# Performance work log

Measured on AMD Instinct MI355X. Metric: run time of the kernel, lower is better.

## Reference

```python
import jax, jax.numpy as jnp
import numpy as np

B, H, S, DK = 4, 8, 2048, 64

def setup_inputs() -> dict:
    key = jax.random.key(0)
    kq, kk, kv = jax.random.split(key, 3)
    queries = jax.random.normal(kq, (B, H, S, DK), dtype=jnp.float32)
    keys = jax.random.normal(kk, (B, H, S, DK), dtype=jnp.float32)
    values = jax.random.normal(kv, (B, H, S, DK), dtype=jnp.float32)
    # causal mask: 1.0 where attention is disallowed (strictly upper triangular)
    mask = jnp.triu(jnp.ones((S, S), dtype=jnp.float32), k=1)[None, None]
    return {"queries": queries, "keys": keys, "values": values, "dk": DK, "mask": mask}

def reference(queries, keys, values, dk, mask):
    # score: [B, H, S, S]
    score = jnp.einsum("bhqd,bhkd->bhqk", queries, keys) / jnp.sqrt(jnp.float32(dk))
    if mask is not None:
        score = score + mask * -1e9
    attn = jax.nn.softmax(score, axis=-1)
    return jnp.einsum("bhqk,bhkd->bhqd", attn, values)
```

## Files before the change

kernel.cpp:

```cpp
#include <hip/hip_runtime.h>

typedef __attribute__((ext_vector_type(8))) short short8;
typedef __attribute__((ext_vector_type(4))) float f32x4;

#define DEV __device__ __forceinline__

constexpr int S_LEN = 2048;
constexpr int DK_LEN = 64;
constexpr int QBLK = 128;
constexpr int KBLK = 64;
constexpr float QSCALE = 0.18033688011112042f;

constexpr int KHI = 0;
constexpr int KLO = 8192;
constexpr int VHI = 16384;
constexpr int VLO = 24576;
constexpr int PBASE = 32768;
constexpr int LDS_BYTES = 65536;

DEV unsigned int f2bf(float x) {
  unsigned int u = __float_as_uint(x);
  return (u + 0x7fffu + ((u >> 16) & 1u)) >> 16;
}
DEV float bf2f(unsigned int h) { return __uint_as_float(h << 16); }
DEV int swz(int row, int slot) { return slot ^ ((row + (row >> 3)) & 7); }

DEV f32x4 MFMA(short8 a, short8 b, f32x4 c) {
  return __builtin_amdgcn_mfma_f32_16x16x32_bf16(a, b, c, 0, 0, 0);
}

__global__ __launch_bounds__(256, 2)
void fattn_fwd(const float* __restrict__ Qg, const float* __restrict__ Kg,
               const float* __restrict__ Vg, float* __restrict__ Og)
{
  __shared__ char smem[LDS_BYTES];
  const f32x4 vzero = {0.f, 0.f, 0.f, 0.f};
  const int tid = threadIdx.x;
  const int w  = tid >> 6;
  const int ln = tid & 63;
  const int g  = ln >> 4;
  const int c  = ln & 15;
  const int bh = blockIdx.y;
  const int qi = (bh < 16) ? (15 - (int)blockIdx.x) : (int)blockIdx.x;
  const int q0w = qi * QBLK + w * 32;
  const size_t base = (size_t)bh * S_LEN * DK_LEN;
  const float* Qb = Qg + base;
  const float* Kb = Kg + base;
  const float* Vb = Vg + base;

  short8 qfh[2][2], qfl[2][2];
#pragma unroll
  for (int qt = 0; qt < 2; ++qt) {
    const float* Qr = Qb + (size_t)(q0w + 16 * qt + c) * DK_LEN;
#pragma unroll
    for (int kk = 0; kk < 2; ++kk) {
      f32x4 a = *(const f32x4*)(Qr + kk * 32 + 8 * g);
      f32x4 b = *(const f32x4*)(Qr + kk * 32 + 8 * g + 4);
      float x[8];
#pragma unroll
      for (int i = 0; i < 4; ++i) { x[i] = a[i] * QSCALE; x[4 + i] = b[i] * QSCALE; }
#pragma unroll
      for (int i = 0; i < 8; ++i) {
        unsigned int h = f2bf(x[i]);
        unsigned int l = f2bf(x[i] - bf2f(h));
        qfh[qt][kk][i] = (short)h;
        qfl[qt][kk][i] = (short)l;
      }
    }
  }

  f32x4 acc[4][2];
#pragma unroll
  for (int td = 0; td < 4; ++td)
#pragma unroll
    for (int qt = 0; qt < 2; ++qt) acc[td][qt] = vzero;
  float m_r[2]  = {-3e38f, -3e38f};
  float lsum[2] = {0.f, 0.f};

  const int ntiles = 2 * qi + 2;
  for (int kt = 0; kt < ntiles; ++kt) {
    const int kv0 = kt * KBLK;
    __syncthreads();
#pragma unroll
    for (int i = 0; i < 4; ++i) {
      int f = tid + 256 * i;
      int row = f >> 4, c4 = f & 15;
      f32x4 kv = *(const f32x4*)(Kb + (size_t)(kv0 + row) * DK_LEN + c4 * 4);
      unsigned int h[4], l[4];
#pragma unroll
      for (int j = 0; j < 4; ++j) { h[j] = f2bf(kv[j]); l[j] = f2bf(kv[j] - bf2f(h[j])); }
      int byte = row * 128 + swz(row, c4 >> 1) * 16 + (c4 & 1) * 8;
      *(uint2*)(smem + KHI + byte) = make_uint2(h[0] | (h[1] << 16), h[2] | (h[3] << 16));
      *(uint2*)(smem + KLO + byte) = make_uint2(l[0] | (l[1] << 16), l[2] | (l[3] << 16));
    }
#pragma unroll
    for (int it = 0; it < 2; ++it) {
      int p = tid + 256 * it;
      int rp = p >> 4, c4 = p & 15;
      const float* vp = Vb + (size_t)(kv0 + 2 * rp) * DK_LEN + c4 * 4;
      f32x4 v0 = *(const f32x4*)(vp);
      f32x4 v1 = *(const f32x4*)(vp + DK_LEN);
#pragma unroll
      for (int j = 0; j < 4; ++j) {
        int d = 4 * c4 + j;
        unsigned int h0 = f2bf(v0[j]), h1 = f2bf(v1[j]);
        unsigned int l0 = f2bf(v0[j] - bf2f(h0)), l1 = f2bf(v1[j] - bf2f(h1));
        int byte = d * 128 + swz(d, rp >> 2) * 16 + (rp & 3) * 4;
        *(unsigned int*)(smem + VHI + byte) = h0 | (h1 << 16);
        *(unsigned int*)(smem + VLO + byte) = l0 | (l1 << 16);
      }
    }
    __syncthreads();

    if (kv0 > q0w + 31) continue;
    const bool need_mask = (kv0 + KBLK - 1) > q0w;

    f32x4 sv[2][4];
#pragma unroll
    for (int qt = 0; qt < 2; ++qt)
#pragma unroll
      for (int t = 0; t < 4; ++t) sv[qt][t] = vzero;
#pragma unroll
    for (int t = 0; t < 4; ++t) {
      int row = 16 * t + c;
#pragma unroll
      for (int kk = 0; kk < 2; ++kk) {
        int off = row * 128 + swz(row, 4 * kk + g) * 16;
        short8 kh = *(const short8*)(smem + KHI + off);
        short8 kl = *(const short8*)(smem + KLO + off);
#pragma unroll
        for (int qt = 0; qt < 2; ++qt) {
          sv[qt][t] = MFMA(kh, qfh[qt][kk], sv[qt][t]);
          sv[qt][t] = MFMA(kh, qfl[qt][kk], sv[qt][t]);
          sv[qt][t] = MFMA(kl, qfh[qt][kk], sv[qt][t]);
        }
      }
    }
    if (need_mask) {
#pragma unroll
      for (int qt = 0; qt < 2; ++qt) {
        int q = q0w + 16 * qt + c;
#pragma unroll
        for (int t = 0; t < 4; ++t)
#pragma unroll
          for (int r = 0; r < 4; ++r)
            if (kv0 + 16 * t + 4 * g + r > q) sv[qt][t][r] = -1e38f;
      }
    }

    char* pw = smem + PBASE + w * 8192;
#pragma unroll
    for (int qt = 0; qt < 2; ++qt) {
      float mt = -3e38f;
#pragma unroll
      for (int t = 0; t < 4; ++t)
#pragma unroll
        for (int r = 0; r < 4; ++r) mt = fmaxf(mt, sv[qt][t][r]);
      mt = fmaxf(mt, __shfl_xor(mt, 16));
      mt = fmaxf(mt, __shfl_xor(mt, 32));
      float mn = fmaxf(m_r[qt], mt);
      float sc = exp2f(m_r[qt] - mn);
      m_r[qt] = mn;
#pragma unroll
      for (int td = 0; td < 4; ++td) acc[td][qt] *= sc;
      float ps = 0.f;
      int qrow = 16 * qt + c;
      char* ph = pw + qrow * 128;
      char* pl = ph + 4096;
#pragma unroll
      for (int t = 0; t < 4; ++t) {
        float p[4];
#pragma unroll
        for (int r = 0; r < 4; ++r) { p[r] = exp2f(sv[qt][t][r] - mn); ps += p[r]; }
        unsigned int h0 = f2bf(p[0]), h1 = f2bf(p[1]), h2 = f2bf(p[2]), h3 = f2bf(p[3]);
        unsigned int l0 = f2bf(p[0] - bf2f(h0)), l1 = f2bf(p[1] - bf2f(h1));
        unsigned int l2 = f2bf(p[2] - bf2f(h2)), l3 = f2bf(p[3] - bf2f(h3));
        int kb = 32 * t + 8 * g;
        int byte = swz(qrow, kb >> 4) * 16 + (kb & 15);
        *(unsigned int*)(ph + byte)     = h0 | (h1 << 16);
        *(unsigned int*)(ph + byte + 4) = h2 | (h3 << 16);
        *(unsigned int*)(pl + byte)     = l0 | (l1 << 16);
        *(unsigned int*)(pl + byte + 4) = l2 | (l3 << 16);
      }
      lsum[qt] = lsum[qt] * sc + ps;
    }

    short8 pbh[2][2], pbl[2][2];
#pragma unroll
    for (int qt = 0; qt < 2; ++qt) {
      int qrow = 16 * qt + c;
#pragma unroll
      for (int kk = 0; kk < 2; ++kk) {
        int off = qrow * 128 + swz(qrow, 4 * kk + g) * 16;
        pbh[qt][kk] = *(const short8*)(pw + off);
        pbl[qt][kk] = *(const short8*)(pw + 4096 + off);
      }
    }
#pragma unroll
    for (int td = 0; td < 4; ++td) {
      int d = 16 * td + c;
#pragma unroll
      for (int kk = 0; kk < 2; ++kk) {
        int off = d * 128 + swz(d, 4 * kk + g) * 16;
        short8 vh = *(const short8*)(smem + VHI + off);
        short8 vl = *(const short8*)(smem + VLO + off);
#pragma unroll
        for (int qt = 0; qt < 2; ++qt) {
          acc[td][qt] = MFMA(vh, pbh[qt][kk], acc[td][qt]);
          acc[td][qt] = MFMA(vh, pbl[qt][kk], acc[td][qt]);
          acc[td][qt] = MFMA(vl, pbh[qt][kk], acc[td][qt]);
        }
      }
    }
  }

#pragma unroll
  for (int qt = 0; qt < 2; ++qt) {
    float l = lsum[qt];
    l += __shfl_xor(l, 16);
    l += __shfl_xor(l, 32);
    float inv = 1.f / l;
    float* Ob = Og + base + (size_t)(q0w + 16 * qt + c) * DK_LEN;
#pragma unroll
    for (int td = 0; td < 4; ++td) {
      f32x4 o = acc[td][qt] * inv;
      *(f32x4*)(Ob + 16 * td + 4 * g) = o;
    }
  }
}

extern "C" void kernel_launch(void* const* d_in, const int* in_sizes, int n_in,
                              void* d_out, int out_size, void* d_ws, size_t ws_size,
                              hipStream_t stream) {
  (void)in_sizes; (void)n_in; (void)d_ws; (void)ws_size; (void)out_size;
  const float* Q = (const float*)d_in[0];
  const float* K = (const float*)d_in[1];
  const float* V = (const float*)d_in[2];
  float* O = (float*)d_out;
  dim3 grid(16, 32);
  fattn_fwd<<<grid, dim3(256), 0, stream>>>(Q, K, V, O);
}
```

Baseline: 209.4 us.

## Pair high and low 64-row query chunks per block for causal balance

Each block now processes two 64-row query chunks, one from the end of the sequence and its mirror from the start, instead of one contiguous 128-row chunk. Every block streams KV tiles up to the high chunk, and MFMA work for the low chunk is skipped once its causal range is passed. The goal is to even out causal work across blocks so no block is left with very few or very many tiles. The cost is more total K/V global loads and bf16 conversions, because low-chunk rows ride along with the long-running high chunk.

```diff
diff --git a/kernel.cpp b/kernel.cpp
--- a/kernel.cpp
+++ b/kernel.cpp
@@ -7,7 +7,6 @@
 
 constexpr int S_LEN = 2048;
 constexpr int DK_LEN = 64;
-constexpr int QBLK = 128;
 constexpr int KBLK = 64;
 constexpr float QSCALE = 0.18033688011112042f;
 
@@ -41,8 +40,12 @@
   const int g  = ln >> 4;
   const int c  = ln & 15;
   const int bh = blockIdx.y;
-  const int qi = (bh < 16) ? (15 - (int)blockIdx.x) : (int)blockIdx.x;
-  const int q0w = qi * QBLK + w * 32;
+  const int j  = blockIdx.x;
+  const int hc = 31 - j;
+  const int lc = j;
+  int qb[2];
+  qb[0] = hc * 64 + 16 * w;
+  qb[1] = lc * 64 + 16 * w;
   const size_t base = (size_t)bh * S_LEN * DK_LEN;
   const float* Qb = Qg + base;
   const float* Kb = Kg + base;
@@ -51,7 +54,7 @@
   short8 qfh[2][2], qfl[2][2];
 #pragma unroll
   for (int qt = 0; qt < 2; ++qt) {
-    const float* Qr = Qb + (size_t)(q0w + 16 * qt + c) * DK_LEN;
+    const float* Qr = Qb + (size_t)(qb[qt] + c) * DK_LEN;
 #pragma unroll
     for (int kk = 0; kk < 2; ++kk) {
       f32x4 a = *(const f32x4*)(Qr + kk * 32 + 8 * g);
@@ -76,8 +79,45 @@
     for (int qt = 0; qt < 2; ++qt) acc[td][qt] = vzero;
   float m_r[2]  = {-3e38f, -3e38f};
   float lsum[2] = {0.f, 0.f};
-
-  const int ntiles = 2 * qi + 2;
+  f32x4 sv[2][4];
+  char* pw = smem + PBASE + w * 8192;
+
+  auto softmax_store = [&](int qt) {
+    float mt = -3e38f;
+#pragma unroll
+    for (int t = 0; t < 4; ++t)
+#pragma unroll
+      for (int r = 0; r < 4; ++r) mt = fmaxf(mt, sv[qt][t][r]);
+    mt = fmaxf(mt, __shfl_xor(mt, 16));
+    mt = fmaxf(mt, __shfl_xor(mt, 32));
+    float mn = fmaxf(m_r[qt], mt);
+    float sc = exp2f(m_r[qt] - mn);
+    m_r[qt] = mn;
+#pragma unroll
+    for (int td = 0; td < 4; ++td) acc[td][qt] *= sc;
+    float ps = 0.f;
+    int qrow = 16 * qt + c;
+    char* ph = pw + qrow * 128;
+    char* pl = ph + 4096;
+#pragma unroll
+    for (int t = 0; t < 4; ++t) {
+      float p[4];
+#pragma unroll
+      for (int r = 0; r < 4; ++r) { p[r] = exp2f(sv[qt][t][r] - mn); ps += p[r]; }
+      unsigned int h0 = f2bf(p[0]), h1 = f2bf(p[1]), h2 = f2bf(p[2]), h3 = f2bf(p[3]);
+      unsigned int l0 = f2bf(p[0] - bf2f(h0)), l1 = f2bf(p[1] - bf2f(h1));
+      unsigned int l2 = f2bf(p[2] - bf2f(h2)), l3 = f2bf(p[3] - bf2f(h3));
+      int kb = 32 * t + 8 * g;
+      int byte = swz(qrow, kb >> 4) * 16 + (kb & 15);
+      *(unsigned int*)(ph + byte)     = h0 | (h1 << 16);
+      *(unsigned int*)(ph + byte + 4) = h2 | (h3 << 16);
+      *(unsigned int*)(pl + byte)     = l0 | (l1 << 16);
+      *(unsigned int*)(pl + byte + 4) = l2 | (l3 << 16);
+    }
+    lsum[qt] = lsum[qt] * sc + ps;
+  };
+
+  const int ntiles = hc + 1;
   for (int kt = 0; kt < ntiles; ++kt) {
     const int kv0 = kt * KBLK;
     __syncthreads();
@@ -88,7 +128,7 @@
       f32x4 kv = *(const f32x4*)(Kb + (size_t)(kv0 + row) * DK_LEN + c4 * 4);
       unsigned int h[4], l[4];
 #pragma unroll
-      for (int j = 0; j < 4; ++j) { h[j] = f2bf(kv[j]); l[j] = f2bf(kv[j] - bf2f(h[j])); }
+      for (int jj = 0; jj < 4; ++jj) { h[jj] = f2bf(kv[jj]); l[jj] = f2bf(kv[jj] - bf2f(h[jj])); }
       int byte = row * 128 + swz(row, c4 >> 1) * 16 + (c4 & 1) * 8;
       *(uint2*)(smem + KHI + byte) = make_uint2(h[0] | (h[1] << 16), h[2] | (h[3] << 16));
       *(uint2*)(smem + KLO + byte) = make_uint2(l[0] | (l[1] << 16), l[2] | (l[3] << 16));
@@ -101,10 +141,10 @@
       f32x4 v0 = *(const f32x4*)(vp);
       f32x4 v1 = *(const f32x4*)(vp + DK_LEN);
 #pragma unroll
-      for (int j = 0; j < 4; ++j) {
-        int d = 4 * c4 + j;
-        unsigned int h0 = f2bf(v0[j]), h1 = f2bf(v1[j]);
-        unsigned int l0 = f2bf(v0[j] - bf2f(h0)), l1 = f2bf(v1[j] - bf2f(h1));
+      for (int jj = 0; jj < 4; ++jj) {
+        int d = 4 * c4 + jj;
+        unsigned int h0 = f2bf(v0[jj]), h1 = f2bf(v1[jj]);
+        unsigned int l0 = f2bf(v0[jj] - bf2f(h0)), l1 = f2bf(v1[jj] - bf2f(h1));
         int byte = d * 128 + swz(d, rp >> 2) * 16 + (rp & 3) * 4;
         *(unsigned int*)(smem + VHI + byte) = h0 | (h1 << 16);
         *(unsigned int*)(smem + VLO + byte) = l0 | (l1 << 16);
@@ -112,10 +152,10 @@
     }
     __syncthreads();
 
-    if (kv0 > q0w + 31) continue;
-    const bool need_mask = (kv0 + KBLK - 1) > q0w;
-
-    f32x4 sv[2][4];
+    const bool act1 = (kv0 <= qb[1] + 15);
+    const bool nm0  = (kv0 + KBLK - 1) > qb[0];
+    const bool nm1  = (kv0 + KBLK - 1) > qb[1];
+
 #pragma unroll
     for (int qt = 0; qt < 2; ++qt)
 #pragma unroll
@@ -128,72 +168,51 @@
         int off = row * 128 + swz(row, 4 * kk + g) * 16;
         short8 kh = *(const short8*)(smem + KHI + off);
         short8 kl = *(const short8*)(smem + KLO + off);
-#pragma unroll
-        for (int qt = 0; qt < 2; ++qt) {
-          sv[qt][t] = MFMA(kh, qfh[qt][kk], sv[qt][t]);
-          sv[qt][t] = MFMA(kh, qfl[qt][kk], sv[qt][t]);
-          sv[qt][t] = MFMA(kl, qfh[qt][kk], sv[qt][t]);
+        sv[0][t] = MFMA(kh, qfh[0][kk], sv[0][t]);
+        sv[0][t] = MFMA(kh, qfl[0][kk], sv[0][t]);
+        sv[0][t] = MFMA(kl, qfh[0][kk], sv[0][t]);
+        if (act1) {
+          sv[1][t] = MFMA(kh, qfh[1][kk], sv[1][t]);
+          sv[1][t] = MFMA(kh, qfl[1][kk], sv[1][t]);
+          sv[1][t] = MFMA(kl, qfh[1][kk], sv[1][t]);
         }
       }
     }
-    if (need_mask) {
-#pragma unroll
-      for (int qt = 0; qt < 2; ++qt) {
-        int q = q0w + 16 * qt + c;
-#pragma unroll
-        for (int t = 0; t < 4; ++t)
-#pragma unroll
-          for (int r = 0; r < 4; ++r)
-            if (kv0 + 16 * t + 4 * g + r > q) sv[qt][t][r] = -1e38f;
-      }
-    }
-
-    char* pw = smem + PBASE + w * 8192;
-#pragma unroll
-    for (int qt = 0; qt < 2; ++qt) {
-      float mt = -3e38f;
+    if (nm0) {
+      int q = qb[0] + c;
 #pragma unroll
       for (int t = 0; t < 4; ++t)
 #pragma unroll
-        for (int r = 0; r < 4; ++r) mt = fmaxf(mt, sv[qt][t][r]);
-      mt = fmaxf(mt, __shfl_xor(mt, 16));
-      mt = fmaxf(mt, __shfl_xor(mt, 32));
-      float mn = fmaxf(m_r[qt], mt);
-      float sc = exp2f(m_r[qt] - mn);
-      m_r[qt] = mn;
-#pragma unroll
-      for (int td = 0; td < 4; ++td) acc[td][qt] *= sc;
-      float ps = 0.f;
-      int qrow = 16 * qt + c;
-      char* ph = pw + qrow * 128;
-      char* pl = ph + 4096;
-#pragma unroll
-      for (int t = 0; t < 4; ++t) {
-        float p[4];
-#pragma unroll
-        for (int r = 0; r < 4; ++r) { p[r] = exp2f(sv[qt][t][r] - mn); ps += p[r]; }
-        unsigned int h0 = f2bf(p[0]), h1 = f2bf(p[1]), h2 = f2bf(p[2]), h3 = f2bf(p[3]);
-        unsigned int l0 = f2bf(p[0] - bf2f(h0)), l1 = f2bf(p[1] - bf2f(h1));
-        unsigned int l2 = f2bf(p[2] - bf2f(h2)), l3 = f2bf(p[3] - bf2f(h3));
-        int kb = 32 * t + 8 * g;
-        int byte = swz(qrow, kb >> 4) * 16 + (kb & 15);
-        *(unsigned int*)(ph + byte)     = h0 | (h1 << 16);
-        *(unsigned int*)(ph + byte + 4) = h2 | (h3 << 16);
-        *(unsigned int*)(pl + byte)     = l0 | (l1 << 16);
-        *(unsigned int*)(pl + byte + 4) = l2 | (l3 << 16);
-      }
-      lsum[qt] = lsum[qt] * sc + ps;
-    }
+        for (int r = 0; r < 4; ++r)
+          if (kv0 + 16 * t + 4 * g + r > q) sv[0][t][r] = -1e38f;
+    }
+    if (act1 && nm1) {
+      int q = qb[1] + c;
+#pragma unroll
+      for (int t = 0; t < 4; ++t)
+#pragma unroll
+        for (int r = 0; r < 4; ++r)
+          if (kv0 + 16 * t + 4 * g + r > q) sv[1][t][r] = -1e38f;
+    }
+
+    softmax_store(0);
+    if (act1) softmax_store(1);
 
     short8 pbh[2][2], pbl[2][2];
 #pragma unroll
-    for (int qt = 0; qt < 2; ++qt) {
-      int qrow = 16 * qt + c;
+    for (int kk = 0; kk < 2; ++kk) {
+      int qrow = c;
+      int off = qrow * 128 + swz(qrow, 4 * kk + g) * 16;
+      pbh[0][kk] = *(const short8*)(pw + off);
+      pbl[0][kk] = *(const short8*)(pw + 4096 + off);
+    }
+    if (act1) {
 #pragma unroll
       for (int kk = 0; kk < 2; ++kk) {
+        int qrow = 16 + c;
         int off = qrow * 128 + swz(qrow, 4 * kk + g) * 16;
-        pbh[qt][kk] = *(const short8*)(pw + off);
-        pbl[qt][kk] = *(const short8*)(pw + 4096 + off);
+        pbh[1][kk] = *(const short8*)(pw + off);
+        pbl[1][kk] = *(const short8*)(pw + 4096 + off);
       }
     }
 #pragma unroll
@@ -204,11 +223,13 @@
         int off = d * 128 + swz(d, 4 * kk + g) * 16;
         short8 vh = *(const short8*)(smem + VHI + off);
         short8 vl = *(const short8*)(smem + VLO + off);
-#pragma unroll
-        for (int qt = 0; qt < 2; ++qt) {
-          acc[td][qt] = MFMA(vh, pbh[qt][kk], acc[td][qt]);
-          acc[td][qt] = MFMA(vh, pbl[qt][kk], acc[td][qt]);
-          acc[td][qt] = MFMA(vl, pbh[qt][kk], acc[td][qt]);
+        acc[td][0] = MFMA(vh, pbh[0][kk], acc[td][0]);
+        acc[td][0] = MFMA(vh, pbl[0][kk], acc[td][0]);
+        acc[td][0] = MFMA(vl, pbh[0][kk], acc[td][0]);
+        if (act1) {
+          acc[td][1] = MFMA(vh, pbh[1][kk], acc[td][1]);
+          acc[td][1] = MFMA(vh, pbl[1][kk], acc[td][1]);
+          acc[td][1] = MFMA(vl, pbh[1][kk], acc[td][1]);
         }
       }
     }
@@ -220,7 +241,7 @@
     l += __shfl_xor(l, 16);
     l += __shfl_xor(l, 32);
     float inv = 1.f / l;
-    float* Ob = Og + base + (size_t)(q0w + 16 * qt + c) * DK_LEN;
+    float* Ob = Og + base + (size_t)(qb[qt] + c) * DK_LEN;
 #pragma unroll
     for (int td = 0; td < 4; ++td) {
       f32x4 o = acc[td][qt] * inv;
```

Measured after the change: 208.7 us. No clear change (-0.4%).
